# Kernel optimization log

Measured on AMD Instinct MI355X. Metric: run time of the kernel, lower is better.

Reference implementation:

```python
import jax, jax.numpy as jnp
import numpy as np
import math

D = 1024
W = 128  # window_size


def _decay_mask(L, gamma, dtype):
    # Diagonal-block LD decay mask: within each window-sized block on the
    # diagonal apply tril(gamma**|i-j|); everywhere else leave attn untouched (1.0).
    i = jnp.arange(L)
    diff = i[:, None] - i[None, :]                     # [L, L] q_idx - k_idx
    same_block = (i[:, None] // W) == (i[None, :] // W)
    safe_exp = jnp.maximum(diff, 0).astype(dtype)      # avoid gamma**(negative)
    in_block = jnp.where(diff >= 0, gamma ** safe_exp, jnp.zeros((), dtype))
    return jnp.where(same_block, in_block, jnp.ones((), dtype))


def setup_inputs() -> dict:
    key = jax.random.key(0)
    ks = jax.random.split(key, 5)
    B, L = 2, 4096
    x = jax.random.normal(ks[0], (B, L, D), dtype=jnp.float32)
    Wqkv = jax.random.normal(ks[1], (D, 3 * D), dtype=jnp.float32) * 0.02
    bqkv = jnp.zeros((3 * D,), dtype=jnp.float32)
    Wproj = jax.random.normal(ks[2], (D, D), dtype=jnp.float32) * 0.02
    bproj = jnp.zeros((D,), dtype=jnp.float32)
    gamma = jnp.float32(0.9)
    return {"x": x, "Wqkv": Wqkv, "bqkv": bqkv, "Wproj": Wproj,
            "bproj": bproj, "gamma": gamma}


def reference(x, Wqkv, bqkv, Wproj, bproj, gamma):
    B, L, d = x.shape
    qkv = x @ Wqkv + bqkv                              # [B, L, 3D]
    q, k, v = jnp.split(qkv, 3, axis=-1)
    attn = jnp.einsum('bqd,bkd->bqk', q, k) / math.sqrt(d)
    mask = _decay_mask(L, gamma, x.dtype)              # [L, L]
    attn = attn * mask[None, :, :]
    attn = jax.nn.softmax(attn, axis=-1)
    out = jnp.einsum('bqk,bkd->bqd', attn, v)
    return out @ Wproj + bproj
```

## Files before the change

### kernel.cpp

```cpp
#include <hip/hip_runtime.h>
#include <math.h>


typedef unsigned short u16;
using short8 = __attribute__((ext_vector_type(8))) short;
using f32x4  = __attribute__((ext_vector_type(4))) float;

typedef __attribute__((address_space(3))) void       lds_void;
typedef const __attribute__((address_space(1))) void glb_void;

__device__ __forceinline__ u16 f2bf(float f) {
    unsigned u = __builtin_bit_cast(unsigned, f);
    unsigned r = u + 0x7fffu + ((u >> 16) & 1u);
    return (u16)(r >> 16);
}

__device__ __forceinline__ void stage_tile(const u16* __restrict__ gsrc, int ld,
                                           int row0, int k0, u16* ltile, int w, int l)
{
#pragma unroll
    for (int i = 0; i < 2; ++i) {
        const int rt = w * 32 + i * 16 + (l >> 2);
        const int s  = l & 3;
        const int g  = s ^ ((rt >> 1) & 3);
        const u16* gp = gsrc + (size_t)(row0 + rt) * ld + k0 + g * 8;
        u16* lp = ltile + (w * 32 + i * 16) * 32;
        __builtin_amdgcn_global_load_lds((glb_void*)gp, (lds_void*)lp, 16, 0, 0);
    }
}

__device__ __forceinline__ short8 frag_read(const u16* tile, int rbase, int lane15, int lg)
{
    const int r = rbase + lane15;
    const int s = lg ^ ((r >> 1) & 3);
    return *(const short8*)(tile + r * 32 + s * 8);
}

template<int EPI, int BIAS>
__global__ __launch_bounds__(256, 2)
void gemm_bt(const u16* __restrict__ A, const u16* __restrict__ Bm,
             const float* __restrict__ bias,
             float* __restrict__ Cf, u16* __restrict__ Cb,
             int M, int N, int K, int lda, int ldb, int ldc,
             int rowOff, float scale, const float* __restrict__ gammaPtr)
{
    __shared__ u16 lds[2][2][128 * 32];

    const int tid = threadIdx.x;
    const int w = tid >> 6, l = tid & 63;
    const int m0 = blockIdx.y * 128, n0 = blockIdx.x * 128;
    const int wr = w >> 1, wc = w & 1;
    const int lane15 = l & 15, lg = l >> 4;

    f32x4 acc[4][4] = {};

    stage_tile(A,  lda, m0, 0, lds[0][0], w, l);
    stage_tile(Bm, ldb, n0, 0, lds[0][1], w, l);
    __syncthreads();

    const int NSTEP = K >> 5;
    for (int kt = 0; kt < NSTEP; ++kt) {
        const int buf = kt & 1;
        if (kt + 1 < NSTEP) {
            const int k1 = (kt + 1) << 5;
            stage_tile(A,  lda, m0, k1, lds[buf ^ 1][0], w, l);
            stage_tile(Bm, ldb, n0, k1, lds[buf ^ 1][1], w, l);
        }
        short8 aF[4], bF[4];
#pragma unroll
        for (int i = 0; i < 4; ++i) {
            aF[i] = frag_read(lds[buf][0], wr * 64 + i * 16, lane15, lg);
            bF[i] = frag_read(lds[buf][1], wc * 64 + i * 16, lane15, lg);
        }
#pragma unroll
        for (int mi = 0; mi < 4; ++mi)
#pragma unroll
            for (int ni = 0; ni < 4; ++ni)
                acc[mi][ni] = __builtin_amdgcn_mfma_f32_16x16x32_bf16(aF[mi], bF[ni], acc[mi][ni], 0, 0, 0);
        __syncthreads();
    }

    const float l2g = (EPI == 2) ? log2f(gammaPtr[0]) : 0.f;
#pragma unroll
    for (int mi = 0; mi < 4; ++mi)
#pragma unroll
        for (int ni = 0; ni < 4; ++ni) {
            const int colg = n0 + wc * 64 + ni * 16 + lane15;
            const float bv = BIAS ? bias[colg] : 0.f;
            const int rbase = m0 + wr * 64 + mi * 16 + lg * 4;
            if (EPI == 3) {
                ushort4 o;
                o.x = f2bf(acc[mi][ni][0] + bv);
                o.y = f2bf(acc[mi][ni][1] + bv);
                o.z = f2bf(acc[mi][ni][2] + bv);
                o.w = f2bf(acc[mi][ni][3] + bv);
                *(ushort4*)&Cb[(size_t)colg * ldc + rbase] = o;
            } else {
#pragma unroll
                for (int t = 0; t < 4; ++t) {
                    const int rowg = rbase + t;
                    float v = acc[mi][ni][t];
                    if (EPI == 2) {
                        v *= scale;
                        const int qg = rowOff + rowg;
                        if ((qg >> 7) == (colg >> 7)) {
                            const int d = qg - colg;
                            v = (d >= 0) ? v * exp2f((float)d * l2g) : 0.f;
                        }
                        Cf[(size_t)rowg * ldc + colg] = v;
                    } else if (EPI == 1) {
                        Cb[(size_t)rowg * ldc + colg] = f2bf(v + bv);
                    } else {
                        Cf[(size_t)rowg * ldc + colg] = v + bv;
                    }
                }
            }
        }
}

__global__ __launch_bounds__(256)
void convert_bf16_vec(const float* __restrict__ in, u16* __restrict__ outp, int n4)
{
    int idx = blockIdx.x * 256 + threadIdx.x;
    const int stride = gridDim.x * 256;
    for (; idx < n4; idx += stride) {
        const float4 v = ((const float4*)in)[idx];
        ushort4 h;
        h.x = f2bf(v.x); h.y = f2bf(v.y); h.z = f2bf(v.z); h.w = f2bf(v.w);
        ((ushort4*)outp)[idx] = h;
    }
}

__global__ __launch_bounds__(256)
void convert_bf16_T(const float* __restrict__ Wm, u16* __restrict__ T, int R, int C)
{
    __shared__ float tf[32][33];
    const int r0 = blockIdx.y * 32, c0 = blockIdx.x * 32;
    const int tr = threadIdx.x >> 3;
    const int tc = (threadIdx.x & 7) * 4;
    const float4 v = *(const float4*)&Wm[(size_t)(r0 + tr) * C + c0 + tc];
    tf[tr][tc + 0] = v.x; tf[tr][tc + 1] = v.y;
    tf[tr][tc + 2] = v.z; tf[tr][tc + 3] = v.w;
    __syncthreads();
    ushort4 h;
    h.x = f2bf(tf[tc + 0][tr]);
    h.y = f2bf(tf[tc + 1][tr]);
    h.z = f2bf(tf[tc + 2][tr]);
    h.w = f2bf(tf[tc + 3][tr]);
    *(ushort4*)&T[(size_t)(c0 + tr) * R + r0 + tc] = h;
}

__global__ __launch_bounds__(256)
void softmax_inplace(float* __restrict__ Sc)
{
    float* p = Sc + (size_t)blockIdx.x * 4096;
    const int tid = threadIdx.x, wid = tid >> 6, lane = tid & 63;

    float4 v[4];
    float mx = -1e30f;
#pragma unroll
    for (int c = 0; c < 4; ++c) {
        v[c] = *(const float4*)&p[c * 1024 + tid * 4];
        mx = fmaxf(mx, fmaxf(fmaxf(v[c].x, v[c].y), fmaxf(v[c].z, v[c].w)));
    }
#pragma unroll
    for (int off = 32; off; off >>= 1) mx = fmaxf(mx, __shfl_xor(mx, off, 64));

    __shared__ float red[8];
    if (lane == 0) red[wid] = mx;
    __syncthreads();
    mx = fmaxf(fmaxf(red[0], red[1]), fmaxf(red[2], red[3]));

    float sum = 0.f;
#pragma unroll
    for (int c = 0; c < 4; ++c) {
        v[c].x = __expf(v[c].x - mx); v[c].y = __expf(v[c].y - mx);
        v[c].z = __expf(v[c].z - mx); v[c].w = __expf(v[c].w - mx);
        sum += v[c].x + v[c].y + v[c].z + v[c].w;
    }
#pragma unroll
    for (int off = 32; off; off >>= 1) sum += __shfl_xor(sum, off, 64);
    if (lane == 0) red[4 + wid] = sum;
    __syncthreads();
    sum = red[4] + red[5] + red[6] + red[7];

    const float inv = 1.f / sum;
    u16* pb = (u16*)p;
#pragma unroll
    for (int c = 0; c < 4; ++c) {
        ushort4 h;
        h.x = f2bf(v[c].x * inv); h.y = f2bf(v[c].y * inv);
        h.z = f2bf(v[c].z * inv); h.w = f2bf(v[c].w * inv);
        *(ushort4*)&pb[c * 1024 + tid * 4] = h;
    }
}

extern "C" void kernel_launch(void* const* d_in, const int* in_sizes, int n_in,
                              void* d_out, int out_size, void* d_ws, size_t ws_size,
                              hipStream_t stream)
{
    const float* x     = (const float*)d_in[0];
    const float* Wqkv  = (const float*)d_in[1];
    const float* bqkv  = (const float*)d_in[2];
    const float* Wproj = (const float*)d_in[3];
    const float* bproj = (const float*)d_in[4];
    const float* gamma = (const float*)d_in[5];
    float* out = (float*)d_out;

    const int B = 2, L = 4096, D = 1024;
    const size_t BASE = 58720256ull;

    int CH = 0;
    for (int c = 4096; c >= 128; c >>= 1)
        if (BASE + (size_t)c * 16384ull <= ws_size) { CH = c; break; }
    if (!CH) return;

    char* ws = (char*)d_ws;
    u16*   WqT = (u16*)(ws);
    u16*   WpT = (u16*)(ws + 6291456);
    u16*   xb  = (u16*)(ws + 8388608);
    u16*   qk  = (u16*)(ws + 25165824);
    u16*   vT  = (u16*)(ws + 41943040);
    u16*   Ob  = (u16*)(ws + 50331648);
    float* S   = (float*)(ws + 58720256);

    convert_bf16_vec<<<2048, 256, 0, stream>>>(x, xb, B * L * D / 4);
    convert_bf16_T<<<dim3(3 * D / 32, D / 32), 256, 0, stream>>>(Wqkv, WqT, D, 3 * D);
    convert_bf16_T<<<dim3(D / 32, D / 32), 256, 0, stream>>>(Wproj, WpT, D, D);

    for (int b = 0; b < B; ++b) {
        const u16* xbb = xb + (size_t)b * L * D;

        gemm_bt<1, 1><<<dim3(16, 32), 256, 0, stream>>>(
            xbb, WqT, bqkv, nullptr, qk,
            L, 2 * D, D, D, D, 2 * D, 0, 1.f, nullptr);

        gemm_bt<3, 1><<<dim3(8, 32), 256, 0, stream>>>(
            xbb, WqT + (size_t)(2 * D) * D, bqkv + 2 * D, nullptr, vT,
            L, D, D, D, D, L, 0, 1.f, nullptr);

        for (int c0 = 0; c0 < L; c0 += CH) {
            gemm_bt<2, 0><<<dim3(32, CH / 128), 256, 0, stream>>>(
                qk + (size_t)c0 * (2 * D), qk + D, nullptr, S, nullptr,
                CH, L, D, 2 * D, 2 * D, L, c0, 0.03125f, gamma);

            softmax_inplace<<<CH, 256, 0, stream>>>(S);

            gemm_bt<1, 0><<<dim3(8, CH / 128), 256, 0, stream>>>(
                (const u16*)S, vT, nullptr, nullptr, Ob + (size_t)c0 * D,
                CH, D, L, 2 * L, L, D, 0, 1.f, nullptr);
        }

        gemm_bt<0, 1><<<dim3(8, 32), 256, 0, stream>>>(
            Ob, WpT, bproj, out + (size_t)b * L * D, nullptr,
            L, D, D, D, D, D, 0, 1.f, nullptr);
    }
}
```

Before: 511.3 us.

## Fuse QKV GEMM, transpose V separately, add XCD block swizzle, separate P buffer

After: 480.3 us. 6.1% less time.

```diff
diff --git a/kernel.cpp b/kernel.cpp
--- a/kernel.cpp
+++ b/kernel.cpp
@@ -48,7 +48,13 @@
 
     const int tid = threadIdx.x;
     const int w = tid >> 6, l = tid & 63;
-    const int m0 = blockIdx.y * 128, n0 = blockIdx.x * 128;
+
+    const int gx  = gridDim.x;
+    const int nwg = gx * gridDim.y;
+    int bid = blockIdx.y * gx + blockIdx.x;
+    if ((nwg & 7) == 0) bid = (bid & 7) * (nwg >> 3) + (bid >> 3);
+    const int m0 = (bid / gx) * 128, n0 = (bid % gx) * 128;
+
     const int wr = w >> 1, wc = w & 1;
     const int lane15 = l & 15, lg = l >> 4;
 
@@ -88,31 +94,22 @@
             const int colg = n0 + wc * 64 + ni * 16 + lane15;
             const float bv = BIAS ? bias[colg] : 0.f;
             const int rbase = m0 + wr * 64 + mi * 16 + lg * 4;
-            if (EPI == 3) {
-                ushort4 o;
-                o.x = f2bf(acc[mi][ni][0] + bv);
-                o.y = f2bf(acc[mi][ni][1] + bv);
-                o.z = f2bf(acc[mi][ni][2] + bv);
-                o.w = f2bf(acc[mi][ni][3] + bv);
-                *(ushort4*)&Cb[(size_t)colg * ldc + rbase] = o;
-            } else {
-#pragma unroll
-                for (int t = 0; t < 4; ++t) {
-                    const int rowg = rbase + t;
-                    float v = acc[mi][ni][t];
-                    if (EPI == 2) {
-                        v *= scale;
-                        const int qg = rowOff + rowg;
-                        if ((qg >> 7) == (colg >> 7)) {
-                            const int d = qg - colg;
-                            v = (d >= 0) ? v * exp2f((float)d * l2g) : 0.f;
-                        }
-                        Cf[(size_t)rowg * ldc + colg] = v;
-                    } else if (EPI == 1) {
-                        Cb[(size_t)rowg * ldc + colg] = f2bf(v + bv);
-                    } else {
-                        Cf[(size_t)rowg * ldc + colg] = v + bv;
+#pragma unroll
+            for (int t = 0; t < 4; ++t) {
+                const int rowg = rbase + t;
+                float v = acc[mi][ni][t];
+                if (EPI == 2) {
+                    v *= scale;
+                    const int qg = rowOff + rowg;
+                    if ((qg >> 7) == (colg >> 7)) {
+                        const int d = qg - colg;
+                        v = (d >= 0) ? v * exp2f((float)d * l2g) : 0.f;
                     }
+                    Cf[(size_t)rowg * ldc + colg] = v;
+                } else if (EPI == 1) {
+                    Cb[(size_t)rowg * ldc + colg] = f2bf(v + bv);
+                } else {
+                    Cf[(size_t)rowg * ldc + colg] = v + bv;
                 }
             }
         }
@@ -151,9 +148,27 @@
 }
 
 __global__ __launch_bounds__(256)
-void softmax_inplace(float* __restrict__ Sc)
-{
-    float* p = Sc + (size_t)blockIdx.x * 4096;
+void transpose_v(const u16* __restrict__ qkv, u16* __restrict__ vT)
+{
+    __shared__ u16 t[32][33];
+    const int c0 = blockIdx.x * 32;
+    const int r0 = blockIdx.y * 32;
+    const int tr = threadIdx.x >> 3;
+    const int tc = (threadIdx.x & 7) * 4;
+    const ushort4 v = *(const ushort4*)&qkv[(size_t)(r0 + tr) * 3072 + 2048 + c0 + tc];
+    t[tr][tc + 0] = v.x; t[tr][tc + 1] = v.y;
+    t[tr][tc + 2] = v.z; t[tr][tc + 3] = v.w;
+    __syncthreads();
+    ushort4 o;
+    o.x = t[tc + 0][tr]; o.y = t[tc + 1][tr];
+    o.z = t[tc + 2][tr]; o.w = t[tc + 3][tr];
+    *(ushort4*)&vT[(size_t)(c0 + tr) * 4096 + r0 + tc] = o;
+}
+
+__global__ __launch_bounds__(256)
+void softmax_rows(const float* __restrict__ S, u16* __restrict__ P)
+{
+    const float* p = S + (size_t)blockIdx.x * 4096;
     const int tid = threadIdx.x, wid = tid >> 6, lane = tid & 63;
 
     float4 v[4];
@@ -185,13 +200,13 @@
     sum = red[4] + red[5] + red[6] + red[7];
 
     const float inv = 1.f / sum;
-    u16* pb = (u16*)p;
+    ushort4* pb4 = (ushort4*)(P + (size_t)blockIdx.x * 4096);
 #pragma unroll
     for (int c = 0; c < 4; ++c) {
         ushort4 h;
         h.x = f2bf(v[c].x * inv); h.y = f2bf(v[c].y * inv);
         h.z = f2bf(v[c].z * inv); h.w = f2bf(v[c].w * inv);
-        *(ushort4*)&pb[c * 1024 + tid * 4] = h;
+        pb4[c * 256 + tid] = h;
     }
 }
 
@@ -212,43 +227,41 @@
 
     int CH = 0;
     for (int c = 4096; c >= 128; c >>= 1)
-        if (BASE + (size_t)c * 16384ull <= ws_size) { CH = c; break; }
+        if (BASE + (size_t)c * 24576ull <= ws_size) { CH = c; break; }
     if (!CH) return;
 
     char* ws = (char*)d_ws;
     u16*   WqT = (u16*)(ws);
     u16*   WpT = (u16*)(ws + 6291456);
     u16*   xb  = (u16*)(ws + 8388608);
-    u16*   qk  = (u16*)(ws + 25165824);
+    u16*   qkv = (u16*)(ws + 16777216);
     u16*   vT  = (u16*)(ws + 41943040);
     u16*   Ob  = (u16*)(ws + 50331648);
     float* S   = (float*)(ws + 58720256);
-
-    convert_bf16_vec<<<2048, 256, 0, stream>>>(x, xb, B * L * D / 4);
+    u16*   P   = (u16*)(ws + 58720256 + (size_t)CH * 16384ull);
+
     convert_bf16_T<<<dim3(3 * D / 32, D / 32), 256, 0, stream>>>(Wqkv, WqT, D, 3 * D);
     convert_bf16_T<<<dim3(D / 32, D / 32), 256, 0, stream>>>(Wproj, WpT, D, D);
 
     for (int b = 0; b < B; ++b) {
-        const u16* xbb = xb + (size_t)b * L * D;
-
-        gemm_bt<1, 1><<<dim3(16, 32), 256, 0, stream>>>(
-            xbb, WqT, bqkv, nullptr, qk,
-            L, 2 * D, D, D, D, 2 * D, 0, 1.f, nullptr);
-
-        gemm_bt<3, 1><<<dim3(8, 32), 256, 0, stream>>>(
-            xbb, WqT + (size_t)(2 * D) * D, bqkv + 2 * D, nullptr, vT,
-            L, D, D, D, D, L, 0, 1.f, nullptr);
+        convert_bf16_vec<<<1024, 256, 0, stream>>>(x + (size_t)b * L * D, xb, L * D / 4);
+
+        gemm_bt<1, 1><<<dim3(24, 32), 256, 0, stream>>>(
+            xb, WqT, bqkv, nullptr, qkv,
+            L, 3 * D, D, D, D, 3 * D, 0, 1.f, nullptr);
+
+        transpose_v<<<dim3(D / 32, L / 32), 256, 0, stream>>>(qkv, vT);
 
         for (int c0 = 0; c0 < L; c0 += CH) {
             gemm_bt<2, 0><<<dim3(32, CH / 128), 256, 0, stream>>>(
-                qk + (size_t)c0 * (2 * D), qk + D, nullptr, S, nullptr,
-                CH, L, D, 2 * D, 2 * D, L, c0, 0.03125f, gamma);
-
-            softmax_inplace<<<CH, 256, 0, stream>>>(S);
+                qkv + (size_t)c0 * (3 * D), qkv + D, nullptr, S, nullptr,
+                CH, L, D, 3 * D, 3 * D, L, c0, 0.03125f, gamma);
+
+            softmax_rows<<<CH, 256, 0, stream>>>(S, P);
 
             gemm_bt<1, 0><<<dim3(8, CH / 128), 256, 0, stream>>>(
-                (const u16*)S, vT, nullptr, nullptr, Ob + (size_t)c0 * D,
-                CH, D, L, 2 * L, L, D, 0, 1.f, nullptr);
+                P, vT, nullptr, nullptr, Ob + (size_t)c0 * D,
+                CH, D, L, L, L, D, 0, 1.f, nullptr);
         }
 
         gemm_bt<0, 1><<<dim3(8, 32), 256, 0, stream>>>(
```
